# Kernel tuning notes

Hardware: AMD Instinct MI355X
Metric: run time of the kernel (lower is better)

The kernel has to match this reference:

```python
import jax, jax.numpy as jnp
import numpy as np

B, L, C = 32, 2048, 32
PL, STRIDE = 16, 16
P = L // PL
D, H_ENC, H_DEC, K, NH = 64, 256, 256, 512, 4
BETA, EPS, Q_EPS, CW = 0.25, 1e-5, 1e-5, 0.2


def setup_inputs() -> dict:
    key = jax.random.key(0)
    ks = jax.random.split(key, 16)
    g = lambda k, sh: 0.02 * jax.random.normal(k, sh, dtype=jnp.float32)
    return {
        'x': jax.random.normal(ks[0], (B, L, C), dtype=jnp.float32),
        'revin_w': jnp.ones((C,), jnp.float32), 'revin_b': jnp.zeros((C,), jnp.float32),
        'inp_W': g(ks[1], (PL, D)), 'inp_b': jnp.zeros((D,), jnp.float32),
        'Wq': g(ks[2], (D, D)), 'bq': jnp.zeros((D,), jnp.float32),
        'Wk': g(ks[3], (D, D)), 'bk': jnp.zeros((D,), jnp.float32),
        'Wv': g(ks[4], (D, D)), 'bv': jnp.zeros((D,), jnp.float32),
        'Wo': g(ks[5], (D, D)), 'bo': jnp.zeros((D,), jnp.float32),
        'ln1_g': jnp.ones((D,), jnp.float32), 'ln1_b': jnp.zeros((D,), jnp.float32),
        'ffn_W1': g(ks[6], (D, H_ENC)), 'ffn_b1': jnp.zeros((H_ENC,), jnp.float32),
        'ffn_W2': g(ks[7], (H_ENC, D)), 'ffn_b2': jnp.zeros((D,), jnp.float32),
        'ln2_g': jnp.ones((D,), jnp.float32), 'ln2_b': jnp.zeros((D,), jnp.float32),
        'codebook': jax.random.uniform(ks[8], (K, D), jnp.float32, -1.0 / K, 1.0 / K),
        'dec_W1': g(ks[9], (D, H_DEC)), 'dec_b1': jnp.zeros((H_DEC,), jnp.float32),
        'dec_W2': g(ks[10], (H_DEC, PL)), 'dec_b2': jnp.zeros((PL,), jnp.float32),
        'dec_Wr': g(ks[11], (D, PL)), 'dec_br': jnp.zeros((PL,), jnp.float32),
        'dec_ln_g': jnp.ones((PL,), jnp.float32), 'dec_ln_b': jnp.zeros((PL,), jnp.float32),
    }


def _layernorm(x, g, b):
    m = jnp.mean(x, -1, keepdims=True)
    v = jnp.mean((x - m) ** 2, -1, keepdims=True)
    return (x - m) * jax.lax.rsqrt(v + EPS) * g + b


def reference(x, revin_w, revin_b, inp_W, inp_b, Wq, bq, Wk, bk, Wv, bv, Wo, bo,
              ln1_g, ln1_b, ffn_W1, ffn_b1, ffn_W2, ffn_b2, ln2_g, ln2_b, codebook,
              dec_W1, dec_b1, dec_W2, dec_b2, dec_Wr, dec_br, dec_ln_g, dec_ln_b):
    # --- RevIN norm (stats over time dim) ---
    mean = jnp.mean(x, axis=1, keepdims=True)              # [B,1,C]
    std = jnp.sqrt(jnp.var(x, axis=1, keepdims=True) + EPS)
    xn = (x - mean) / std * revin_w + revin_b
    # --- patchify: [B,C,L] -> [B*C, P, PL] ---
    patches = jnp.transpose(xn, (0, 2, 1)).reshape(B * C, P, PL)
    # --- MHEncoder ---
    h = patches @ inp_W + inp_b                            # [N,P,D]
    dh = D // NH
    q = (h @ Wq + bq).reshape(-1, P, NH, dh)
    k = (h @ Wk + bk).reshape(-1, P, NH, dh)
    v = (h @ Wv + bv).reshape(-1, P, NH, dh)
    scores = jnp.einsum('nqhd,nkhd->nhqk', q, k) / np.sqrt(dh).astype(np.float32)
    attn = jax.nn.softmax(scores, axis=-1)
    a = jnp.einsum('nhqk,nkhd->nqhd', attn, v).reshape(-1, P, D)
    a = a @ Wo + bo
    h = _layernorm(h + a, ln1_g, ln1_b)
    ff = jax.nn.relu(h @ ffn_W1 + ffn_b1) @ ffn_W2 + ffn_b2
    h = _layernorm(h + ff, ln2_g, ln2_b)
    z = h.reshape(B, C, P, D)
    # --- ClusterQuantizer ---
    z2 = jnp.sum(z * z, -1, keepdims=True)                 # [B,V,P,1]
    e2 = jnp.sum(codebook * codebook, -1)                  # [K]
    ze = jnp.einsum('bvpd,kd->bvpk', z, codebook)
    dist = z2 + e2 - 2.0 * ze                              # [B,V,P,K]
    indices = jnp.argmin(dist, axis=-1)                    # [B,V,P] int
    z_q = codebook[indices]
    z_q_st = z + jax.lax.stop_gradient(z_q - z)
    codebook_loss = jnp.mean((z_q - jax.lax.stop_gradient(z)) ** 2)
    commitment_loss = jnp.mean((z - jax.lax.stop_gradient(z_q)) ** 2)
    cluster_loss = codebook_loss + BETA * commitment_loss
    counts = jnp.zeros((K,), jnp.float32).at[indices.ravel()].add(1.0)
    probs = counts / (counts.sum() + EPS)
    perplexity = jnp.exp(-jnp.sum(probs * jnp.log(probs + EPS)))
    # --- FFN decoder ---
    y = jax.nn.relu(z_q_st @ dec_W1 + dec_b1) @ dec_W2 + dec_b2
    y = y + z_q_st @ dec_Wr + dec_br
    recon_patches = _layernorm(y, dec_ln_g, dec_ln_b)      # [B,V,P,PL]
    recon = jnp.transpose(recon_patches.reshape(B, C, L), (0, 2, 1))  # [B,L,C]
    # --- RevIN denorm ---
    r = (recon - revin_b) / (revin_w + EPS * EPS) * std + mean
    rec_loss = jnp.mean((x - r) ** 2)
    loss_total = rec_loss + CW * cluster_loss
    return (loss_total, rec_loss, z_q_st, r, indices, perplexity)
```

## Files before the change

### kernel.cpp

```cpp
#include <hip/hip_runtime.h>
#include <math.h>

#define TPB 256

#define B_  32
#define L_  2048
#define C_  32
#define PL_ 16
#define P_  128
#define D_  64
#define HE_ 256
#define HD_ 256
#define K_  512
#define N_  1024
#define M_  131072

#define EPS_  1e-5f
#define BETA_ 0.25f
#define CW_   0.2f

#define OUT_LOSS 0
#define OUT_REC  1
#define OUT_ZQ   2
#define OUT_R    8388610
#define OUT_IDX  10485762
#define OUT_PERP 10616834

#define WS_MEAN   0
#define WS_STD    1024
#define WS_QT     2048
#define WS_KT     6144
#define WS_VT     10240
#define WS_E2     34816
#define WS_COUNTS 35328
#define WS_CPART  35840
#define WS_H0     36864
#define WS_H1     8425472
#define WS_RPART  WS_H1

__global__ void k_prep(const float* __restrict__ Wq, const float* __restrict__ Wk,
                       const float* __restrict__ Wv,
                       const float* __restrict__ cb, float* __restrict__ ws) {
    int g = blockIdx.x * TPB + threadIdx.x;
    if (g < 4096) { int t = g >> 6, j = g & 63; ws[WS_QT + g] = Wq[j * D_ + t]; }
    else if (g < 8192) { int g2 = g - 4096; int t = g2 >> 6, j = g2 & 63; ws[WS_KT + g2] = Wk[j * D_ + t]; }
    else if (g < 12288) { int g2 = g - 8192; int t = g2 >> 6, j = g2 & 63; ws[WS_VT + g2] = Wv[j * D_ + t]; }
    if (g < K_) {
        float s = 0.f;
        for (int j = 0; j < D_; j++) { float v = cb[g * D_ + j]; s += v * v; }
        ws[WS_E2 + g] = s;
    }
}

__global__ void k_stats(const float* __restrict__ x, float* __restrict__ ws) {
    const int blk = blockIdx.x;
    const int b = blk >> 3, c0 = (blk & 7) * 4;
    const float4* xp = (const float4*)(x + (size_t)b * L_ * C_ + c0);
    float4 s = {0.f, 0.f, 0.f, 0.f}, s2 = {0.f, 0.f, 0.f, 0.f};
    for (int l = threadIdx.x; l < L_; l += TPB) {
        float4 v = xp[(size_t)l * 8];
        s.x += v.x; s.y += v.y; s.z += v.z; s.w += v.w;
        s2.x += v.x * v.x; s2.y += v.y * v.y; s2.z += v.z * v.z; s2.w += v.w * v.w;
    }
    __shared__ float4 sh[TPB], sh2[TPB];
    sh[threadIdx.x] = s; sh2[threadIdx.x] = s2; __syncthreads();
    for (int o2 = 128; o2 > 0; o2 >>= 1) {
        if (threadIdx.x < o2) {
            float4 a = sh[threadIdx.x], bq_ = sh[threadIdx.x + o2];
            a.x += bq_.x; a.y += bq_.y; a.z += bq_.z; a.w += bq_.w; sh[threadIdx.x] = a;
            float4 a2 = sh2[threadIdx.x], b2_ = sh2[threadIdx.x + o2];
            a2.x += b2_.x; a2.y += b2_.y; a2.z += b2_.z; a2.w += b2_.w; sh2[threadIdx.x] = a2;
        }
        __syncthreads();
    }
    if (threadIdx.x == 0) {
        float sv[4] = {sh[0].x, sh[0].y, sh[0].z, sh[0].w};
        float qv[4] = {sh2[0].x, sh2[0].y, sh2[0].z, sh2[0].w};
#pragma unroll
        for (int u = 0; u < 4; u++) {
            float m = sv[u] / (float)L_;
            float var = qv[u] / (float)L_ - m * m;
            ws[WS_MEAN + b * 32 + c0 + u] = m;
            ws[WS_STD + b * 32 + c0 + u] = sqrtf(var + EPS_);
        }
    }
}

__global__ __launch_bounds__(TPB) void k_embed(
    const float* __restrict__ x, const float* __restrict__ rw, const float* __restrict__ rb,
    const float* __restrict__ inpW, const float* __restrict__ inpb, float* __restrict__ ws) {
    int g = blockIdx.x * TPB + threadIdx.x;
    int row = g >> 4, d4 = g & 15;
    int n = row >> 7, p = row & 127;
    int b = n >> 5, c = n & 31;
    float m = ws[WS_MEAN + n], sd = ws[WS_STD + n];
    float w = rw[c], bb = rb[c];
    const float* xp = x + (size_t)b * L_ * C_ + (size_t)p * PL_ * C_ + c;
    const float4* W4 = (const float4*)inpW;
    float4 acc = ((const float4*)inpb)[d4];
#pragma unroll
    for (int j = 0; j < PL_; j++) {
        float xv = xp[(size_t)j * C_];
        float xn = (xv - m) / sd * w + bb;
        float4 wv = W4[j * 16 + d4];
        acc.x += xn * wv.x; acc.y += xn * wv.y; acc.z += xn * wv.z; acc.w += xn * wv.w;
    }
    ((float4*)(ws + WS_H0))[g] = acc;
}

#define HSS  68
#define HS_  0
#define KH_  8704
#define VH_  10752
#define SMF  12800

__global__ __launch_bounds__(TPB) void k_attn(
    float* __restrict__ ws,
    const float* __restrict__ bq, const float* __restrict__ bk, const float* __restrict__ bv) {
    __shared__ float sm[SMF];
    const int tid = threadIdx.x;
    const int xcd = blockIdx.x & 7, iw = blockIdx.x >> 3;
    const int n = xcd * 128 + (iw >> 2), hh = iw & 3;
    const float* h0 = ws + WS_H0 + (size_t)n * (P_ * D_);
    float* agl = ws + WS_H1 + (size_t)n * (P_ * D_);

    {
        const float4* h04 = (const float4*)h0;
#pragma unroll
        for (int it = 0; it < 8; ++it) {
            int e = tid + it * 256;
            int r = e >> 4, j4 = e & 15;
            *(float4*)(sm + HS_ + r * HSS + j4 * 4) = h04[e];
        }
    }
    __syncthreads();

    const int t_ = tid & 15, ib = tid >> 4;
    const float4* WqT4 = (const float4*)(ws + WS_QT);
    const float4* WkT4 = (const float4*)(ws + WS_KT);
    const float4* WvT4 = (const float4*)(ws + WS_VT);

    {
        float4 wk[16], wv[16];
        const float4* kr = WkT4 + (size_t)(hh * 16 + t_) * 16;
        const float4* vr = WvT4 + (size_t)(hh * 16 + t_) * 16;
#pragma unroll
        for (int j4 = 0; j4 < 16; j4++) { wk[j4] = kr[j4]; wv[j4] = vr[j4]; }
        float bbk = bk[hh * 16 + t_], bbv = bv[hh * 16 + t_];
#pragma unroll
        for (int it = 0; it < 8; it++) {
            int i2 = ib + it * 16;
            const float4* hr = (const float4*)(sm + HS_ + i2 * HSS);
            float accK = bbk, accV = bbv;
#pragma unroll
            for (int j4 = 0; j4 < 16; j4++) {
                float4 h4 = hr[j4];
                float4 k4 = wk[j4], v4 = wv[j4];
                accK += h4.x * k4.x + h4.y * k4.y + h4.z * k4.z + h4.w * k4.w;
                accV += h4.x * v4.x + h4.y * v4.y + h4.z * v4.z + h4.w * v4.w;
            }
            sm[KH_ + i2 * 16 + t_] = accK;
            sm[VH_ + i2 * 16 + t_] = accV;
        }
    }
    const int rg = tid >> 2, qt = tid & 3;
    const int rmine = qt >> 1, hmine = qt & 1;
    float qA[16], qB[16];
    {
        const int myrow = rg * 2 + rmine;
        float4 hreg[16];
        const float4* hr = (const float4*)(sm + HS_ + myrow * HSS);
#pragma unroll
        for (int j4 = 0; j4 < 16; j4++) hreg[j4] = hr[j4];
        float qh[8];
#pragma unroll
        for (int u = 0; u < 8; u++) {
            const float4* wr = WqT4 + (size_t)(hh * 16 + hmine * 8 + u) * 16;
            float acc = bq[hh * 16 + hmine * 8 + u];
#pragma unroll
            for (int j4 = 0; j4 < 16; j4++) {
                float4 w4 = wr[j4];
                acc += hreg[j4].x * w4.x + hreg[j4].y * w4.y + hreg[j4].z * w4.z + hreg[j4].w * w4.w;
            }
            qh[u] = acc;
        }
        float qm[16];
#pragma unroll
        for (int u = 0; u < 8; u++) {
            float oth = __shfl_xor(qh[u], 1);
            qm[u] = hmine ? oth : qh[u];
            qm[8 + u] = hmine ? qh[u] : oth;
        }
#pragma unroll
        for (int u = 0; u < 16; u++) {
            float oth = __shfl_xor(qm[u], 2);
            qA[u] = rmine ? oth : qm[u];
            qB[u] = rmine ? qm[u] : oth;
        }
    }
    __syncthreads();
    float SA = 0.f, SB = 0.f;
    float oA[16], oB[16];
#pragma unroll
    for (int u = 0; u < 16; u++) { oA[u] = 0.f; oB[u] = 0.f; }
    const float4* kh4 = (const float4*)(sm + KH_);
    const float4* vh4 = (const float4*)(sm + VH_);
#pragma unroll 4
    for (int k = 0; k < 32; k++) {
        int m = k * 4 + qt;
        float4 a0 = kh4[m * 4 + 0], a1 = kh4[m * 4 + 1], a2 = kh4[m * 4 + 2], a3 = kh4[m * 4 + 3];
        float sA = qA[0] * a0.x + qA[1] * a0.y + qA[2] * a0.z + qA[3] * a0.w
                 + qA[4] * a1.x + qA[5] * a1.y + qA[6] * a1.z + qA[7] * a1.w
                 + qA[8] * a2.x + qA[9] * a2.y + qA[10] * a2.z + qA[11] * a2.w
                 + qA[12] * a3.x + qA[13] * a3.y + qA[14] * a3.z + qA[15] * a3.w;
        float sB = qB[0] * a0.x + qB[1] * a0.y + qB[2] * a0.z + qB[3] * a0.w
                 + qB[4] * a1.x + qB[5] * a1.y + qB[6] * a1.z + qB[7] * a1.w
                 + qB[8] * a2.x + qB[9] * a2.y + qB[10] * a2.z + qB[11] * a2.w
                 + qB[12] * a3.x + qB[13] * a3.y + qB[14] * a3.z + qB[15] * a3.w;
        float pA = __expf(sA * 0.25f);
        float pB = __expf(sB * 0.25f);
        SA += pA; SB += pB;
        float4 v0 = vh4[m * 4 + 0], v1 = vh4[m * 4 + 1], v2 = vh4[m * 4 + 2], v3 = vh4[m * 4 + 3];
        oA[0] += pA * v0.x; oA[1] += pA * v0.y; oA[2] += pA * v0.z; oA[3] += pA * v0.w;
        oA[4] += pA * v1.x; oA[5] += pA * v1.y; oA[6] += pA * v1.z; oA[7] += pA * v1.w;
        oA[8] += pA * v2.x; oA[9] += pA * v2.y; oA[10] += pA * v2.z; oA[11] += pA * v2.w;
        oA[12] += pA * v3.x; oA[13] += pA * v3.y; oA[14] += pA * v3.z; oA[15] += pA * v3.w;
        oB[0] += pB * v0.x; oB[1] += pB * v0.y; oB[2] += pB * v0.z; oB[3] += pB * v0.w;
        oB[4] += pB * v1.x; oB[5] += pB * v1.y; oB[6] += pB * v1.z; oB[7] += pB * v1.w;
        oB[8] += pB * v2.x; oB[9] += pB * v2.y; oB[10] += pB * v2.z; oB[11] += pB * v2.w;
        oB[12] += pB * v3.x; oB[13] += pB * v3.y; oB[14] += pB * v3.z; oB[15] += pB * v3.w;
    }
    {
        SA += __shfl_xor(SA, 1); SA += __shfl_xor(SA, 2);
        SB += __shfl_xor(SB, 1); SB += __shfl_xor(SB, 2);
        float invA = 1.f / SA, invB = 1.f / SB;
#pragma unroll
        for (int u = 0; u < 16; u++) {
            oA[u] += __shfl_xor(oA[u], 1); oA[u] += __shfl_xor(oA[u], 2);
            oB[u] += __shfl_xor(oB[u], 1); oB[u] += __shfl_xor(oB[u], 2);
        }
        const int myrow = rg * 2 + rmine;
        float inv = rmine ? invB : invA;
        float wv[8];
#pragma unroll
        for (int u = 0; u < 8; u++) {
            float va = oA[hmine * 8 + u], vb = oB[hmine * 8 + u];
            wv[u] = (rmine ? vb : va) * inv;
        }
        float4 r0, r1;
        r0.x = wv[0]; r0.y = wv[1]; r0.z = wv[2]; r0.w = wv[3];
        r1.x = wv[4]; r1.y = wv[5]; r1.z = wv[6]; r1.w = wv[7];
        float4* ap4 = (float4*)(agl + (size_t)myrow * D_ + hh * 16 + hmine * 8);
        ap4[0] = r0; ap4[1] = r1;
    }
}

#define FHS  68

__global__ __launch_bounds__(TPB) void k_woffn(
    float* __restrict__ ws, const float* __restrict__ Wo, const float* __restrict__ bo,
    const float* __restrict__ g1, const float* __restrict__ b1,
    const float* __restrict__ fW1, const float* __restrict__ fb1,
    const float* __restrict__ fW2, const float* __restrict__ fb2,
    const float* __restrict__ g2, const float* __restrict__ b2) {
    __shared__ float bufA[64][FHS];
    __shared__ float hT[64][FHS];
    const int tid = threadIdx.x;
    const int row0 = blockIdx.x * 64;
    const float* aog = ws + WS_H1 + (size_t)row0 * D_;

    {
        const float4* ao4 = (const float4*)aog;
#pragma unroll
        for (int it = 0; it < 4; ++it) {
            int e = tid + it * 256;
            int r = e >> 4, j4 = e & 15;
            float4 v = ao4[e];
            bufA[j4 * 4 + 0][r] = v.x; bufA[j4 * 4 + 1][r] = v.y;
            bufA[j4 * 4 + 2][r] = v.z; bufA[j4 * 4 + 3][r] = v.w;
        }
    }
    const int ty = tid >> 4, tx = tid & 15;
    float acc[4][4];
    {
        float4 bb = ((const float4*)bo)[tx];
#pragma unroll
        for (int r = 0; r < 4; r++) { acc[r][0] = bb.x; acc[r][1] = bb.y; acc[r][2] = bb.z; acc[r][3] = bb.w; }
    }
    __syncthreads();
    const float4* Wo4 = (const float4*)Wo;
#pragma unroll 4
    for (int j = 0; j < 64; ++j) {
        float4 a = *(const float4*)&bufA[j][ty * 4];
        float4 w = Wo4[j * 16 + tx];
        float ar[4] = {a.x, a.y, a.z, a.w}, wr[4] = {w.x, w.y, w.z, w.w};
#pragma unroll
        for (int r = 0; r < 4; r++)
#pragma unroll
            for (int c = 0; c < 4; c++) acc[r][c] += ar[r] * wr[c];
    }
    float h1v[4][4];
    {
        const float4* h04 = (const float4*)(ws + WS_H0 + (size_t)row0 * D_);
        float4 gg = ((const float4*)g1)[tx], bbn = ((const float4*)b1)[tx];
#pragma unroll
        for (int r = 0; r < 4; r++) {
            float4 res = h04[(ty * 4 + r) * 16 + tx];
            acc[r][0] += res.x; acc[r][1] += res.y; acc[r][2] += res.z; acc[r][3] += res.w;
            float s = acc[r][0] + acc[r][1] + acc[r][2] + acc[r][3];
            s += __shfl_xor(s, 1); s += __shfl_xor(s, 2); s += __shfl_xor(s, 4); s += __shfl_xor(s, 8);
            float mean_ = s * (1.f / 64.f);
            float vv = 0.f;
#pragma unroll
            for (int c = 0; c < 4; c++) { float d_ = acc[r][c] - mean_; vv += d_ * d_; }
            vv += __shfl_xor(vv, 1); vv += __shfl_xor(vv, 2); vv += __shfl_xor(vv, 4); vv += __shfl_xor(vv, 8);
            float rstd = 1.f / sqrtf(vv * (1.f / 64.f) + EPS_);
            h1v[r][0] = (acc[r][0] - mean_) * rstd * gg.x + bbn.x;
            h1v[r][1] = (acc[r][1] - mean_) * rstd * gg.y + bbn.y;
            h1v[r][2] = (acc[r][2] - mean_) * rstd * gg.z + bbn.z;
            h1v[r][3] = (acc[r][3] - mean_) * rstd * gg.w + bbn.w;
        }
    }
#pragma unroll
    for (int r = 0; r < 4; r++)
#pragma unroll
        for (int c = 0; c < 4; c++) hT[tx * 4 + c][ty * 4 + r] = h1v[r][c];
    const float4* W14 = (const float4*)fW1;
    const float4* W24 = (const float4*)fW2;
    float outv[4][4];
    {
        float4 bb = ((const float4*)fb2)[tx];
#pragma unroll
        for (int r = 0; r < 4; r++) { outv[r][0] = bb.x; outv[r][1] = bb.y; outv[r][2] = bb.z; outv[r][3] = bb.w; }
    }
    __syncthreads();

    for (int tc = 0; tc < 4; ++tc) {
        float a2[4][4];
        {
            float4 bb1 = ((const float4*)fb1)[tc * 16 + tx];
#pragma unroll
            for (int r = 0; r < 4; r++) { a2[r][0] = bb1.x; a2[r][1] = bb1.y; a2[r][2] = bb1.z; a2[r][3] = bb1.w; }
        }
#pragma unroll 4
        for (int j = 0; j < 64; ++j) {
            float4 a = *(const float4*)&hT[j][ty * 4];
            float4 w = W14[j * 64 + tc * 16 + tx];
            float ar[4] = {a.x, a.y, a.z, a.w}, wr[4] = {w.x, w.y, w.z, w.w};
#pragma unroll
            for (int r = 0; r < 4; r++)
#pragma unroll
                for (int c = 0; c < 4; c++) a2[r][c] += ar[r] * wr[c];
        }
        __syncthreads();
#pragma unroll
        for (int r = 0; r < 4; r++)
#pragma unroll
            for (int c = 0; c < 4; c++) bufA[tx * 4 + c][ty * 4 + r] = fmaxf(a2[r][c], 0.f);
        __syncthreads();
#pragma unroll 4
        for (int h = 0; h < 64; ++h) {
            float4 a = *(const float4*)&bufA[h][ty * 4];
            float4 w = W24[(tc * 64 + h) * 16 + tx];
            float ar[4] = {a.x, a.y, a.z, a.w}, wr[4] = {w.x, w.y, w.z, w.w};
#pragma unroll
            for (int r = 0; r < 4; r++)
#pragma unroll
                for (int c = 0; c < 4; c++) outv[r][c] += ar[r] * wr[c];
        }
    }
    {
        float4 gg = ((const float4*)g2)[tx], bb = ((const float4*)b2)[tx];
        float4* zp = (float4*)(ws + WS_H0 + (size_t)row0 * D_);
#pragma unroll
        for (int r = 0; r < 4; r++) {
            outv[r][0] += h1v[r][0]; outv[r][1] += h1v[r][1];
            outv[r][2] += h1v[r][2]; outv[r][3] += h1v[r][3];
            float s = outv[r][0] + outv[r][1] + outv[r][2] + outv[r][3];
            s += __shfl_xor(s, 1); s += __shfl_xor(s, 2); s += __shfl_xor(s, 4); s += __shfl_xor(s, 8);
            float mean_ = s * (1.f / 64.f);
            float vv = 0.f;
#pragma unroll
            for (int c = 0; c < 4; c++) { float d_ = outv[r][c] - mean_; vv += d_ * d_; }
            vv += __shfl_xor(vv, 1); vv += __shfl_xor(vv, 2); vv += __shfl_xor(vv, 4); vv += __shfl_xor(vv, 8);
            float rstd = 1.f / sqrtf(vv * (1.f / 64.f) + EPS_);
            float4 z;
            z.x = (outv[r][0] - mean_) * rstd * gg.x + bb.x;
            z.y = (outv[r][1] - mean_) * rstd * gg.y + bb.y;
            z.z = (outv[r][2] - mean_) * rstd * gg.z + bb.z;
            z.w = (outv[r][3] - mean_) * rstd * gg.w + bb.w;
            zp[(ty * 4 + r) * 16 + tx] = z;
        }
    }
}

#define QROWS 128
#define QKT   64
#define ZTS   132
#define CBS   68

__global__ __launch_bounds__(TPB) void k_quant(
    float* __restrict__ ws, const float* __restrict__ cb, float* __restrict__ out) {
    __shared__ float zT[64][ZTS];
    __shared__ float cbT[64][CBS];
    __shared__ float z2s[QROWS];
    __shared__ float e2t[QKT];
    __shared__ int   ridx[QROWS];
    __shared__ float red[TPB];

    const int tid = threadIdx.x;
    const int row0 = blockIdx.x * QROWS;
    const float* zg = ws + WS_H0 + (size_t)row0 * D_;
    const float4* zg4 = (const float4*)zg;
    const float4* cbg4 = (const float4*)cb;

    {
        int j4 = tid >> 4;
#pragma unroll
        for (int it = 0; it < 8; ++it) {
            int r = (tid & 15) + it * 16;
            float4 v = zg4[r * 16 + j4];
            zT[j4 * 4 + 0][r] = v.x; zT[j4 * 4 + 1][r] = v.y;
            zT[j4 * 4 + 2][r] = v.z; zT[j4 * 4 + 3][r] = v.w;
        }
    }
    if (tid < QROWS) {
        const float4* zr = (const float4*)(zg + (size_t)tid * D_);
        float s = 0.f;
#pragma unroll
        for (int j = 0; j < 16; j++) { float4 v = zr[j]; s += v.x * v.x + v.y * v.y + v.z * v.z + v.w * v.w; }
        z2s[tid] = s;
    }

    const int ty = tid >> 4, tx = tid & 15;
    float best[8]; int bidx[8];
#pragma unroll
    for (int u = 0; u < 8; u++) { best[u] = 3.4e38f; bidx[u] = 0; }

    for (int t = 0; t < K_ / QKT; ++t) {
        const int k0 = t * QKT;
        __syncthreads();
        {
            int j4 = tid >> 4;
#pragma unroll
            for (int it = 0; it < 4; ++it) {
                int kk = (tid & 15) + it * 16;
                float4 v = cbg4[(size_t)(k0 + kk) * 16 + j4];
                cbT[j4 * 4 + 0][kk] = v.x; cbT[j4 * 4 + 1][kk] = v.y;
                cbT[j4 * 4 + 2][kk] = v.z; cbT[j4 * 4 + 3][kk] = v.w;
            }
        }
        if (tid < QKT) e2t[tid] = ws[WS_E2 + k0 + tid];
        __syncthreads();

        float acc[8][4];
#pragma unroll
        for (int u = 0; u < 8; u++)
#pragma unroll
            for (int c = 0; c < 4; c++) acc[u][c] = 0.f;

        for (int j = 0; j < 64; ++j) {
            float4 a0 = *(const float4*)&zT[j][ty * 8];
            float4 a1 = *(const float4*)&zT[j][ty * 8 + 4];
            float4 b0 = *(const float4*)&cbT[j][tx * 4];
            float ar[8] = {a0.x, a0.y, a0.z, a0.w, a1.x, a1.y, a1.z, a1.w};
            float br[4] = {b0.x, b0.y, b0.z, b0.w};
#pragma unroll
            for (int u = 0; u < 8; u++)
#pragma unroll
                for (int c = 0; c < 4; c++) acc[u][c] += ar[u] * br[c];
        }

#pragma unroll
        for (int u = 0; u < 8; u++) {
            float z2v = z2s[ty * 8 + u];
#pragma unroll
            for (int c = 0; c < 4; c++) {
                float dist = (z2v + e2t[tx * 4 + c]) - 2.f * acc[u][c];
                int kidx = k0 + tx * 4 + c;
                if (dist < best[u]) { best[u] = dist; bidx[u] = kidx; }
            }
        }
    }

#pragma unroll
    for (int m = 1; m <= 8; m <<= 1) {
#pragma unroll
        for (int u = 0; u < 8; u++) {
            float ob = __shfl_xor(best[u], m, 64);
            int oi = __shfl_xor(bidx[u], m, 64);
            if (ob < best[u] || (ob == best[u] && oi < bidx[u])) { best[u] = ob; bidx[u] = oi; }
        }
    }
    if (tx == 0) {
#pragma unroll
        for (int u = 0; u < 8; u++) ridx[ty * 8 + u] = bidx[u];
    }
    __syncthreads();

    if (tid < QROWS) {
        int bi = ridx[tid];
        out[OUT_IDX + row0 + tid] = (float)bi;
        atomicAdd((unsigned int*)ws + WS_COUNTS + bi, 1u);
    }
    {
        int r = tid >> 1, half = tid & 1;
        int bi = ridx[r];
        const float4* cw = (const float4*)(cb + (size_t)bi * D_ + half * 32);
        const float4* zr4 = (const float4*)(zg + (size_t)r * D_ + half * 32);
        float2* zqo = (float2*)(out + OUT_ZQ + (size_t)(row0 + r) * D_ + half * 32);
        float csum = 0.f;
#pragma unroll
        for (int j4 = 0; j4 < 8; ++j4) {
            float4 w = cw[j4]; float4 zz = zr4[j4];
            float d0 = w.x - zz.x, d1 = w.y - zz.y, d2 = w.z - zz.z, d3 = w.w - zz.w;
            csum += d0 * d0 + d1 * d1 + d2 * d2 + d3 * d3;
            float2 p0; p0.x = w.x; p0.y = w.y; zqo[j4 * 2] = p0;
            float2 p1; p1.x = w.z; p1.y = w.w; zqo[j4 * 2 + 1] = p1;
        }
        red[tid] = csum;
    }
    __syncthreads();
    for (int o2 = 128; o2 > 0; o2 >>= 1) {
        if (tid < o2) red[tid] += red[tid + o2];
        __syncthreads();
    }
    if (tid == 0) ws[WS_CPART + blockIdx.x] = red[0];
}

#define DR_ 64

__global__ __launch_bounds__(TPB) void k_dec(
    float* __restrict__ ws, const float* __restrict__ x, const float* __restrict__ cb,
    const float* __restrict__ dW1, const float* __restrict__ db1,
    const float* __restrict__ dW2, const float* __restrict__ db2,
    const float* __restrict__ dWr, const float* __restrict__ dbr,
    const float* __restrict__ lng, const float* __restrict__ lnb,
    const float* __restrict__ rw, const float* __restrict__ rb,
    float* __restrict__ out) {
    __shared__ float zqT[64][FHS];
    __shared__ float Hc[64][FHS];
    __shared__ int   ridx[DR_];
    __shared__ float red[TPB];
    const int tid = threadIdx.x;
    const int row0 = blockIdx.x * DR_;
    if (tid < DR_) ridx[tid] = (int)out[OUT_IDX + row0 + tid];
    __syncthreads();
    {
        const float4* cb4 = (const float4*)cb;
#pragma unroll
        for (int it = 0; it < 4; ++it) {
            int e = tid + it * 256;
            int r = e >> 4, j4 = e & 15;
            float4 v = cb4[(size_t)ridx[r] * 16 + j4];
            zqT[j4 * 4 + 0][r] = v.x; zqT[j4 * 4 + 1][r] = v.y;
            zqT[j4 * 4 + 2][r] = v.z; zqT[j4 * 4 + 3][r] = v.w;
        }
    }
    const int ty = tid >> 4, tx = tid & 15;
    const float4* dW14 = (const float4*)dW1;
    float out4[4];
    {
        float b0 = db2[tx] + dbr[tx];
#pragma unroll
        for (int r = 0; r < 4; r++) out4[r] = b0;
    }
    __syncthreads();

    for (int tc = 0; tc < 4; ++tc) {
        float acc[4][4];
        {
            float4 bb1 = ((const float4*)db1)[tc * 16 + tx];
#pragma unroll
            for (int r = 0; r < 4; r++) { acc[r][0] = bb1.x; acc[r][1] = bb1.y; acc[r][2] = bb1.z; acc[r][3] = bb1.w; }
        }
#pragma unroll 4
        for (int j = 0; j < 64; ++j) {
            float4 a = *(const float4*)&zqT[j][ty * 4];
            float4 w = dW14[j * 64 + tc * 16 + tx];
            float ar[4] = {a.x, a.y, a.z, a.w}, wr[4] = {w.x, w.y, w.z, w.w};
#pragma unroll
            for (int r = 0; r < 4; r++)
#pragma unroll
                for (int c = 0; c < 4; c++) acc[r][c] += ar[r] * wr[c];
        }
        __syncthreads();
#pragma unroll
        for (int r = 0; r < 4; r++)
#pragma unroll
            for (int c = 0; c < 4; c++) Hc[tx * 4 + c][ty * 4 + r] = fmaxf(acc[r][c], 0.f);
        __syncthreads();
#pragma unroll 8
        for (int h = 0; h < 64; ++h) {
            float4 a = *(const float4*)&Hc[h][ty * 4];
            float w = dW2[(tc * 64 + h) * 16 + tx];
            out4[0] += a.x * w; out4[1] += a.y * w; out4[2] += a.z * w; out4[3] += a.w * w;
        }
    }
#pragma unroll 8
    for (int j = 0; j < 64; ++j) {
        float4 a = *(const float4*)&zqT[j][ty * 4];
        float w = dWr[j * 16 + tx];
        out4[0] += a.x * w; out4[1] += a.y * w; out4[2] += a.z * w; out4[3] += a.w * w;
    }
    const int n = row0 >> 7;
    const int b = n >> 5, c = n & 31;
    const float sd = ws[WS_STD + n], mn = ws[WS_MEAN + n];
    const float inv = 1.f / (rw[c] + EPS_ * EPS_);
    const float rbc = rb[c];
    const float lg = lng[tx], lb = lnb[tx];
    float part = 0.f;
#pragma unroll
    for (int r = 0; r < 4; r++) {
        float v = out4[r];
        float s = v;
        s += __shfl_xor(s, 1); s += __shfl_xor(s, 2); s += __shfl_xor(s, 4); s += __shfl_xor(s, 8);
        float mean_ = s * (1.f / 16.f);
        float d_ = v - mean_;
        float vv = d_ * d_;
        vv += __shfl_xor(vv, 1); vv += __shfl_xor(vv, 2); vv += __shfl_xor(vv, 4); vv += __shfl_xor(vv, 8);
        float rstd = 1.f / sqrtf(vv * (1.f / 16.f) + EPS_);
        float yv = d_ * rstd * lg + lb;
        float rr = (yv - rbc) * inv * sd + mn;
        int row = row0 + ty * 4 + r;
        int p = row & 127;
        size_t xi = (size_t)b * L_ * C_ + (size_t)(p * PL_ + tx) * C_ + c;
        out[OUT_R + xi] = rr;
        float dx = x[xi] - rr; part += dx * dx;
    }
    red[tid] = part;
    __syncthreads();
    for (int o2 = 128; o2 > 0; o2 >>= 1) {
        if (tid < o2) red[tid] += red[tid + o2];
        __syncthreads();
    }
    if (tid == 0) ws[WS_RPART + blockIdx.x] = red[0];
}

__global__ void k_final(float* __restrict__ ws, float* __restrict__ out) {
    __shared__ float sh[TPB];
    int tid = threadIdx.x;
    float cs = 0.f;
    for (int i2 = tid; i2 < 1024; i2 += TPB) cs += ws[WS_CPART + i2];
    sh[tid] = cs; __syncthreads();
    for (int o2 = 128; o2 > 0; o2 >>= 1) { if (tid < o2) sh[tid] += sh[tid + o2]; __syncthreads(); }
    float csum = sh[0]; __syncthreads();
    float rs = 0.f;
    for (int i2 = tid; i2 < 2048; i2 += TPB) rs += ws[WS_RPART + i2];
    sh[tid] = rs; __syncthreads();
    for (int o2 = 128; o2 > 0; o2 >>= 1) { if (tid < o2) sh[tid] += sh[tid + o2]; __syncthreads(); }
    float rsum = sh[0]; __syncthreads();
    const unsigned int* counts = (const unsigned int*)ws + WS_COUNTS;
    float H = 0.f;
    for (int k2 = tid; k2 < K_; k2 += TPB) {
        float p = (float)counts[k2] / (131072.f + EPS_);
        H += p * logf(p + EPS_);
    }
    sh[tid] = H; __syncthreads();
    for (int o2 = 128; o2 > 0; o2 >>= 1) { if (tid < o2) sh[tid] += sh[tid + o2]; __syncthreads(); }
    if (tid == 0) {
        float rec = rsum / 2097152.f;
        float msd = csum / 8388608.f;
        float cl = (1.f + BETA_) * msd;
        out[OUT_LOSS] = rec + CW_ * cl;
        out[OUT_REC] = rec;
        out[OUT_PERP] = expf(-sh[0]);
    }
}

extern "C" void kernel_launch(void* const* d_in, const int* in_sizes, int n_in,
                              void* d_out, int out_size, void* d_ws, size_t ws_size,
                              hipStream_t stream) {
    const float* x    = (const float*)d_in[0];
    const float* rw   = (const float*)d_in[1];
    const float* rb   = (const float*)d_in[2];
    const float* inpW = (const float*)d_in[3];
    const float* inpb = (const float*)d_in[4];
    const float* Wq   = (const float*)d_in[5];
    const float* bq   = (const float*)d_in[6];
    const float* Wk   = (const float*)d_in[7];
    const float* bk   = (const float*)d_in[8];
    const float* Wv   = (const float*)d_in[9];
    const float* bv   = (const float*)d_in[10];
    const float* Wo   = (const float*)d_in[11];
    const float* bo   = (const float*)d_in[12];
    const float* g1   = (const float*)d_in[13];
    const float* b1   = (const float*)d_in[14];
    const float* fW1  = (const float*)d_in[15];
    const float* fb1  = (const float*)d_in[16];
    const float* fW2  = (const float*)d_in[17];
    const float* fb2  = (const float*)d_in[18];
    const float* g2   = (const float*)d_in[19];
    const float* b2   = (const float*)d_in[20];
    const float* cb   = (const float*)d_in[21];
    const float* dW1  = (const float*)d_in[22];
    const float* db1  = (const float*)d_in[23];
    const float* dW2  = (const float*)d_in[24];
    const float* db2  = (const float*)d_in[25];
    const float* dWr  = (const float*)d_in[26];
    const float* dbr  = (const float*)d_in[27];
    const float* lng  = (const float*)d_in[28];
    const float* lnb  = (const float*)d_in[29];
    float* ws  = (float*)d_ws;
    float* out = (float*)d_out;

    hipMemsetAsync((char*)d_ws + (size_t)WS_COUNTS * 4, 0, 512 * 4, stream);
    k_prep<<<48, TPB, 0, stream>>>(Wq, Wk, Wv, cb, ws);
    k_stats<<<256, TPB, 0, stream>>>(x, ws);
    k_embed<<<(M_ * 16) / TPB, TPB, 0, stream>>>(x, rw, rb, inpW, inpb, ws);
    k_attn<<<N_ * 4, TPB, 0, stream>>>(ws, bq, bk, bv);
    k_woffn<<<M_ / 64, TPB, 0, stream>>>(ws, Wo, bo, g1, b1, fW1, fb1, fW2, fb2, g2, b2);
    k_quant<<<M_ / QROWS, TPB, 0, stream>>>(ws, cb, out);
    k_dec<<<M_ / DR_, TPB, 0, stream>>>(ws, x, cb, dW1, db1, dW2, db2, dWr, dbr, lng, lnb, rw, rb, out);
    k_final<<<1, TPB, 0, stream>>>(ws, out);
}
```

Baseline: 660.0 us.

## Fuse vector quantization into Wo/FFN kernel and process two heads per attention block

Vector quantization now runs at the end of the Wo/FFN/LayerNorm kernel. The normalized z is kept transposed in shared memory and its squared norms are computed in registers, so z is no longer written to global memory and read back by a separate quant kernel. Each attention block now handles two heads in a loop, so the staged h0 tile in shared memory is reused and half as many blocks are launched. The fused quant uses 64-row tiles, so the codebook is streamed twice as often in total. Codebook-loss partials move to the now-unused transposed-Wq workspace region, and the final reduction sums 2048 partials.

```diff
diff --git a/kernel.cpp b/kernel.cpp
--- a/kernel.cpp
+++ b/kernel.cpp
@@ -33,10 +33,10 @@
 #define WS_VT     10240
 #define WS_E2     34816
 #define WS_COUNTS 35328
-#define WS_CPART  35840
 #define WS_H0     36864
 #define WS_H1     8425472
 #define WS_RPART  WS_H1
+#define WS_CPART2 WS_QT
 
 __global__ void k_prep(const float* __restrict__ Wq, const float* __restrict__ Wk,
                        const float* __restrict__ Wv,
@@ -120,7 +120,7 @@
     __shared__ float sm[SMF];
     const int tid = threadIdx.x;
     const int xcd = blockIdx.x & 7, iw = blockIdx.x >> 3;
-    const int n = xcd * 128 + (iw >> 2), hh = iw & 3;
+    const int n = xcd * 128 + (iw >> 1), hp = iw & 1;
     const float* h0 = ws + WS_H0 + (size_t)n * (P_ * D_);
     float* agl = ws + WS_H1 + (size_t)n * (P_ * D_);
 
@@ -136,135 +136,142 @@
     __syncthreads();
 
     const int t_ = tid & 15, ib = tid >> 4;
+    const int rg = tid >> 2, qt = tid & 3;
+    const int rmine = qt >> 1, hmine = qt & 1;
     const float4* WqT4 = (const float4*)(ws + WS_QT);
     const float4* WkT4 = (const float4*)(ws + WS_KT);
     const float4* WvT4 = (const float4*)(ws + WS_VT);
 
-    {
-        float4 wk[16], wv[16];
-        const float4* kr = WkT4 + (size_t)(hh * 16 + t_) * 16;
-        const float4* vr = WvT4 + (size_t)(hh * 16 + t_) * 16;
-#pragma unroll
-        for (int j4 = 0; j4 < 16; j4++) { wk[j4] = kr[j4]; wv[j4] = vr[j4]; }
-        float bbk = bk[hh * 16 + t_], bbv = bv[hh * 16 + t_];
-#pragma unroll
-        for (int it = 0; it < 8; it++) {
-            int i2 = ib + it * 16;
-            const float4* hr = (const float4*)(sm + HS_ + i2 * HSS);
-            float accK = bbk, accV = bbv;
-#pragma unroll
-            for (int j4 = 0; j4 < 16; j4++) {
-                float4 h4 = hr[j4];
-                float4 k4 = wk[j4], v4 = wv[j4];
-                accK += h4.x * k4.x + h4.y * k4.y + h4.z * k4.z + h4.w * k4.w;
-                accV += h4.x * v4.x + h4.y * v4.y + h4.z * v4.z + h4.w * v4.w;
-            }
-            sm[KH_ + i2 * 16 + t_] = accK;
-            sm[VH_ + i2 * 16 + t_] = accV;
-        }
-    }
-    const int rg = tid >> 2, qt = tid & 3;
-    const int rmine = qt >> 1, hmine = qt & 1;
-    float qA[16], qB[16];
-    {
-        const int myrow = rg * 2 + rmine;
-        float4 hreg[16];
-        const float4* hr = (const float4*)(sm + HS_ + myrow * HSS);
-#pragma unroll
-        for (int j4 = 0; j4 < 16; j4++) hreg[j4] = hr[j4];
-        float qh[8];
-#pragma unroll
-        for (int u = 0; u < 8; u++) {
-            const float4* wr = WqT4 + (size_t)(hh * 16 + hmine * 8 + u) * 16;
-            float acc = bq[hh * 16 + hmine * 8 + u];
-#pragma unroll
-            for (int j4 = 0; j4 < 16; j4++) {
-                float4 w4 = wr[j4];
-                acc += hreg[j4].x * w4.x + hreg[j4].y * w4.y + hreg[j4].z * w4.z + hreg[j4].w * w4.w;
-            }
-            qh[u] = acc;
-        }
-        float qm[16];
-#pragma unroll
-        for (int u = 0; u < 8; u++) {
-            float oth = __shfl_xor(qh[u], 1);
-            qm[u] = hmine ? oth : qh[u];
-            qm[8 + u] = hmine ? qh[u] : oth;
-        }
-#pragma unroll
-        for (int u = 0; u < 16; u++) {
-            float oth = __shfl_xor(qm[u], 2);
-            qA[u] = rmine ? oth : qm[u];
-            qB[u] = rmine ? qm[u] : oth;
-        }
-    }
-    __syncthreads();
-    float SA = 0.f, SB = 0.f;
-    float oA[16], oB[16];
-#pragma unroll
-    for (int u = 0; u < 16; u++) { oA[u] = 0.f; oB[u] = 0.f; }
-    const float4* kh4 = (const float4*)(sm + KH_);
-    const float4* vh4 = (const float4*)(sm + VH_);
+    for (int hl = 0; hl < 2; hl++) {
+        const int hh = hp * 2 + hl;
+        if (hl) __syncthreads();
+        {
+            float4 wk[16], wv[16];
+            const float4* kr = WkT4 + (size_t)(hh * 16 + t_) * 16;
+            const float4* vr = WvT4 + (size_t)(hh * 16 + t_) * 16;
+#pragma unroll
+            for (int j4 = 0; j4 < 16; j4++) { wk[j4] = kr[j4]; wv[j4] = vr[j4]; }
+            float bbk = bk[hh * 16 + t_], bbv = bv[hh * 16 + t_];
+#pragma unroll
+            for (int it = 0; it < 8; it++) {
+                int i2 = ib + it * 16;
+                const float4* hr = (const float4*)(sm + HS_ + i2 * HSS);
+                float accK = bbk, accV = bbv;
+#pragma unroll
+                for (int j4 = 0; j4 < 16; j4++) {
+                    float4 h4 = hr[j4];
+                    float4 k4 = wk[j4], v4 = wv[j4];
+                    accK += h4.x * k4.x + h4.y * k4.y + h4.z * k4.z + h4.w * k4.w;
+                    accV += h4.x * v4.x + h4.y * v4.y + h4.z * v4.z + h4.w * v4.w;
+                }
+                sm[KH_ + i2 * 16 + t_] = accK;
+                sm[VH_ + i2 * 16 + t_] = accV;
+            }
+        }
+        float qA[16], qB[16];
+        {
+            const int myrow = rg * 2 + rmine;
+            float4 hreg[16];
+            const float4* hr = (const float4*)(sm + HS_ + myrow * HSS);
+#pragma unroll
+            for (int j4 = 0; j4 < 16; j4++) hreg[j4] = hr[j4];
+            float qh[8];
+#pragma unroll
+            for (int u = 0; u < 8; u++) {
+                const float4* wr = WqT4 + (size_t)(hh * 16 + hmine * 8 + u) * 16;
+                float acc = bq[hh * 16 + hmine * 8 + u];
+#pragma unroll
+                for (int j4 = 0; j4 < 16; j4++) {
+                    float4 w4 = wr[j4];
+                    acc += hreg[j4].x * w4.x + hreg[j4].y * w4.y + hreg[j4].z * w4.z + hreg[j4].w * w4.w;
+                }
+                qh[u] = acc;
+            }
+            float qm[16];
+#pragma unroll
+            for (int u = 0; u < 8; u++) {
+                float oth = __shfl_xor(qh[u], 1);
+                qm[u] = hmine ? oth : qh[u];
+                qm[8 + u] = hmine ? qh[u] : oth;
+            }
+#pragma unroll
+            for (int u = 0; u < 16; u++) {
+                float oth = __shfl_xor(qm[u], 2);
+                qA[u] = rmine ? oth : qm[u];
+                qB[u] = rmine ? qm[u] : oth;
+            }
+        }
+        __syncthreads();
+        float SA = 0.f, SB = 0.f;
+        float oA[16], oB[16];
+#pragma unroll
+        for (int u = 0; u < 16; u++) { oA[u] = 0.f; oB[u] = 0.f; }
+        const float4* kh4 = (const float4*)(sm + KH_);
+        const float4* vh4 = (const float4*)(sm + VH_);
 #pragma unroll 4
-    for (int k = 0; k < 32; k++) {
-        int m = k * 4 + qt;
-        float4 a0 = kh4[m * 4 + 0], a1 = kh4[m * 4 + 1], a2 = kh4[m * 4 + 2], a3 = kh4[m * 4 + 3];
-        float sA = qA[0] * a0.x + qA[1] * a0.y + qA[2] * a0.z + qA[3] * a0.w
-                 + qA[4] * a1.x + qA[5] * a1.y + qA[6] * a1.z + qA[7] * a1.w
-                 + qA[8] * a2.x + qA[9] * a2.y + qA[10] * a2.z + qA[11] * a2.w
-                 + qA[12] * a3.x + qA[13] * a3.y + qA[14] * a3.z + qA[15] * a3.w;
-        float sB = qB[0] * a0.x + qB[1] * a0.y + qB[2] * a0.z + qB[3] * a0.w
-                 + qB[4] * a1.x + qB[5] * a1.y + qB[6] * a1.z + qB[7] * a1.w
-                 + qB[8] * a2.x + qB[9] * a2.y + qB[10] * a2.z + qB[11] * a2.w
-                 + qB[12] * a3.x + qB[13] * a3.y + qB[14] * a3.z + qB[15] * a3.w;
-        float pA = __expf(sA * 0.25f);
-        float pB = __expf(sB * 0.25f);
-        SA += pA; SB += pB;
-        float4 v0 = vh4[m * 4 + 0], v1 = vh4[m * 4 + 1], v2 = vh4[m * 4 + 2], v3 = vh4[m * 4 + 3];
-        oA[0] += pA * v0.x; oA[1] += pA * v0.y; oA[2] += pA * v0.z; oA[3] += pA * v0.w;
-        oA[4] += pA * v1.x; oA[5] += pA * v1.y; oA[6] += pA * v1.z; oA[7] += pA * v1.w;
-        oA[8] += pA * v2.x; oA[9] += pA * v2.y; oA[10] += pA * v2.z; oA[11] += pA * v2.w;
-        oA[12] += pA * v3.x; oA[13] += pA * v3.y; oA[14] += pA * v3.z; oA[15] += pA * v3.w;
-        oB[0] += pB * v0.x; oB[1] += pB * v0.y; oB[2] += pB * v0.z; oB[3] += pB * v0.w;
-        oB[4] += pB * v1.x; oB[5] += pB * v1.y; oB[6] += pB * v1.z; oB[7] += pB * v1.w;
-        oB[8] += pB * v2.x; oB[9] += pB * v2.y; oB[10] += pB * v2.z; oB[11] += pB * v2.w;
-        oB[12] += pB * v3.x; oB[13] += pB * v3.y; oB[14] += pB * v3.z; oB[15] += pB * v3.w;
-    }
-    {
-        SA += __shfl_xor(SA, 1); SA += __shfl_xor(SA, 2);
-        SB += __shfl_xor(SB, 1); SB += __shfl_xor(SB, 2);
-        float invA = 1.f / SA, invB = 1.f / SB;
-#pragma unroll
-        for (int u = 0; u < 16; u++) {
-            oA[u] += __shfl_xor(oA[u], 1); oA[u] += __shfl_xor(oA[u], 2);
-            oB[u] += __shfl_xor(oB[u], 1); oB[u] += __shfl_xor(oB[u], 2);
-        }
-        const int myrow = rg * 2 + rmine;
-        float inv = rmine ? invB : invA;
-        float wv[8];
-#pragma unroll
-        for (int u = 0; u < 8; u++) {
-            float va = oA[hmine * 8 + u], vb = oB[hmine * 8 + u];
-            wv[u] = (rmine ? vb : va) * inv;
-        }
-        float4 r0, r1;
-        r0.x = wv[0]; r0.y = wv[1]; r0.z = wv[2]; r0.w = wv[3];
-        r1.x = wv[4]; r1.y = wv[5]; r1.z = wv[6]; r1.w = wv[7];
-        float4* ap4 = (float4*)(agl + (size_t)myrow * D_ + hh * 16 + hmine * 8);
-        ap4[0] = r0; ap4[1] = r1;
+        for (int k = 0; k < 32; k++) {
+            int m = k * 4 + qt;
+            float4 a0 = kh4[m * 4 + 0], a1 = kh4[m * 4 + 1], a2 = kh4[m * 4 + 2], a3 = kh4[m * 4 + 3];
+            float sA = qA[0] * a0.x + qA[1] * a0.y + qA[2] * a0.z + qA[3] * a0.w
+                     + qA[4] * a1.x + qA[5] * a1.y + qA[6] * a1.z + qA[7] * a1.w
+                     + qA[8] * a2.x + qA[9] * a2.y + qA[10] * a2.z + qA[11] * a2.w
+                     + qA[12] * a3.x + qA[13] * a3.y + qA[14] * a3.z + qA[15] * a3.w;
+            float sB = qB[0] * a0.x + qB[1] * a0.y + qB[2] * a0.z + qB[3] * a0.w
+                     + qB[4] * a1.x + qB[5] * a1.y + qB[6] * a1.z + qB[7] * a1.w
+                     + qB[8] * a2.x + qB[9] * a2.y + qB[10] * a2.z + qB[11] * a2.w
+                     + qB[12] * a3.x + qB[13] * a3.y + qB[14] * a3.z + qB[15] * a3.w;
+            float pA = __expf(sA * 0.25f);
+            float pB = __expf(sB * 0.25f);
+            SA += pA; SB += pB;
+            float4 v0 = vh4[m * 4 + 0], v1 = vh4[m * 4 + 1], v2 = vh4[m * 4 + 2], v3 = vh4[m * 4 + 3];
+            oA[0] += pA * v0.x; oA[1] += pA * v0.y; oA[2] += pA * v0.z; oA[3] += pA * v0.w;
+            oA[4] += pA * v1.x; oA[5] += pA * v1.y; oA[6] += pA * v1.z; oA[7] += pA * v1.w;
+            oA[8] += pA * v2.x; oA[9] += pA * v2.y; oA[10] += pA * v2.z; oA[11] += pA * v2.w;
+            oA[12] += pA * v3.x; oA[13] += pA * v3.y; oA[14] += pA * v3.z; oA[15] += pA * v3.w;
+            oB[0] += pB * v0.x; oB[1] += pB * v0.y; oB[2] += pB * v0.z; oB[3] += pB * v0.w;
+            oB[4] += pB * v1.x; oB[5] += pB * v1.y; oB[6] += pB * v1.z; oB[7] += pB * v1.w;
+            oB[8] += pB * v2.x; oB[9] += pB * v2.y; oB[10] += pB * v2.z; oB[11] += pB * v2.w;
+            oB[12] += pB * v3.x; oB[13] += pB * v3.y; oB[14] += pB * v3.z; oB[15] += pB * v3.w;
+        }
+        {
+            SA += __shfl_xor(SA, 1); SA += __shfl_xor(SA, 2);
+            SB += __shfl_xor(SB, 1); SB += __shfl_xor(SB, 2);
+            float invA = 1.f / SA, invB = 1.f / SB;
+#pragma unroll
+            for (int u = 0; u < 16; u++) {
+                oA[u] += __shfl_xor(oA[u], 1); oA[u] += __shfl_xor(oA[u], 2);
+                oB[u] += __shfl_xor(oB[u], 1); oB[u] += __shfl_xor(oB[u], 2);
+            }
+            const int myrow = rg * 2 + rmine;
+            float inv = rmine ? invB : invA;
+            float wv[8];
+#pragma unroll
+            for (int u = 0; u < 8; u++) {
+                float va = oA[hmine * 8 + u], vb = oB[hmine * 8 + u];
+                wv[u] = (rmine ? vb : va) * inv;
+            }
+            float4 r0, r1;
+            r0.x = wv[0]; r0.y = wv[1]; r0.z = wv[2]; r0.w = wv[3];
+            r1.x = wv[4]; r1.y = wv[5]; r1.z = wv[6]; r1.w = wv[7];
+            float4* ap4 = (float4*)(agl + (size_t)myrow * D_ + hh * 16 + hmine * 8);
+            ap4[0] = r0; ap4[1] = r1;
+        }
     }
 }
 
 #define FHS  68
 
-__global__ __launch_bounds__(TPB) void k_woffn(
+__global__ __launch_bounds__(TPB) void k_wfq(
     float* __restrict__ ws, const float* __restrict__ Wo, const float* __restrict__ bo,
     const float* __restrict__ g1, const float* __restrict__ b1,
     const float* __restrict__ fW1, const float* __restrict__ fb1,
     const float* __restrict__ fW2, const float* __restrict__ fb2,
-    const float* __restrict__ g2, const float* __restrict__ b2) {
+    const float* __restrict__ g2, const float* __restrict__ b2,
+    const float* __restrict__ cb, float* __restrict__ out) {
     __shared__ float bufA[64][FHS];
     __shared__ float hT[64][FHS];
+    __shared__ int   ridx[64];
+    __shared__ float red[TPB];
     const int tid = threadIdx.x;
     const int row0 = blockIdx.x * 64;
     const float* aog = ws + WS_H1 + (size_t)row0 * D_;
@@ -369,9 +376,9 @@
                 for (int c = 0; c < 4; c++) outv[r][c] += ar[r] * wr[c];
         }
     }
+    float z2r[4];
     {
         float4 gg = ((const float4*)g2)[tx], bb = ((const float4*)b2)[tx];
-        float4* zp = (float4*)(ws + WS_H0 + (size_t)row0 * D_);
 #pragma unroll
         for (int r = 0; r < 4; r++) {
             outv[r][0] += h1v[r][0]; outv[r][1] += h1v[r][1];
@@ -384,61 +391,26 @@
             for (int c = 0; c < 4; c++) { float d_ = outv[r][c] - mean_; vv += d_ * d_; }
             vv += __shfl_xor(vv, 1); vv += __shfl_xor(vv, 2); vv += __shfl_xor(vv, 4); vv += __shfl_xor(vv, 8);
             float rstd = 1.f / sqrtf(vv * (1.f / 64.f) + EPS_);
-            float4 z;
-            z.x = (outv[r][0] - mean_) * rstd * gg.x + bb.x;
-            z.y = (outv[r][1] - mean_) * rstd * gg.y + bb.y;
-            z.z = (outv[r][2] - mean_) * rstd * gg.z + bb.z;
-            z.w = (outv[r][3] - mean_) * rstd * gg.w + bb.w;
-            zp[(ty * 4 + r) * 16 + tx] = z;
-        }
-    }
-}
-
-#define QROWS 128
-#define QKT   64
-#define ZTS   132
-#define CBS   68
-
-__global__ __launch_bounds__(TPB) void k_quant(
-    float* __restrict__ ws, const float* __restrict__ cb, float* __restrict__ out) {
-    __shared__ float zT[64][ZTS];
-    __shared__ float cbT[64][CBS];
-    __shared__ float z2s[QROWS];
-    __shared__ float e2t[QKT];
-    __shared__ int   ridx[QROWS];
-    __shared__ float red[TPB];
-
-    const int tid = threadIdx.x;
-    const int row0 = blockIdx.x * QROWS;
-    const float* zg = ws + WS_H0 + (size_t)row0 * D_;
-    const float4* zg4 = (const float4*)zg;
+            float z0 = (outv[r][0] - mean_) * rstd * gg.x + bb.x;
+            float z1 = (outv[r][1] - mean_) * rstd * gg.y + bb.y;
+            float z2_ = (outv[r][2] - mean_) * rstd * gg.z + bb.z;
+            float z3 = (outv[r][3] - mean_) * rstd * gg.w + bb.w;
+            hT[tx * 4 + 0][ty * 4 + r] = z0;
+            hT[tx * 4 + 1][ty * 4 + r] = z1;
+            hT[tx * 4 + 2][ty * 4 + r] = z2_;
+            hT[tx * 4 + 3][ty * 4 + r] = z3;
+            float zs = z0 * z0 + z1 * z1 + z2_ * z2_ + z3 * z3;
+            zs += __shfl_xor(zs, 1); zs += __shfl_xor(zs, 2); zs += __shfl_xor(zs, 4); zs += __shfl_xor(zs, 8);
+            z2r[r] = zs;
+        }
+    }
     const float4* cbg4 = (const float4*)cb;
-
-    {
-        int j4 = tid >> 4;
-#pragma unroll
-        for (int it = 0; it < 8; ++it) {
-            int r = (tid & 15) + it * 16;
-            float4 v = zg4[r * 16 + j4];
-            zT[j4 * 4 + 0][r] = v.x; zT[j4 * 4 + 1][r] = v.y;
-            zT[j4 * 4 + 2][r] = v.z; zT[j4 * 4 + 3][r] = v.w;
-        }
-    }
-    if (tid < QROWS) {
-        const float4* zr = (const float4*)(zg + (size_t)tid * D_);
-        float s = 0.f;
-#pragma unroll
-        for (int j = 0; j < 16; j++) { float4 v = zr[j]; s += v.x * v.x + v.y * v.y + v.z * v.z + v.w * v.w; }
-        z2s[tid] = s;
-    }
-
-    const int ty = tid >> 4, tx = tid & 15;
-    float best[8]; int bidx[8];
-#pragma unroll
-    for (int u = 0; u < 8; u++) { best[u] = 3.4e38f; bidx[u] = 0; }
-
-    for (int t = 0; t < K_ / QKT; ++t) {
-        const int k0 = t * QKT;
+    float best[4]; int bidx[4];
+#pragma unroll
+    for (int u = 0; u < 4; u++) { best[u] = 3.4e38f; bidx[u] = 0; }
+
+    for (int t = 0; t < 8; ++t) {
+        const int k0 = t * 64;
         __syncthreads();
         {
             int j4 = tid >> 4;
@@ -446,47 +418,43 @@
             for (int it = 0; it < 4; ++it) {
                 int kk = (tid & 15) + it * 16;
                 float4 v = cbg4[(size_t)(k0 + kk) * 16 + j4];
-                cbT[j4 * 4 + 0][kk] = v.x; cbT[j4 * 4 + 1][kk] = v.y;
-                cbT[j4 * 4 + 2][kk] = v.z; cbT[j4 * 4 + 3][kk] = v.w;
-            }
-        }
-        if (tid < QKT) e2t[tid] = ws[WS_E2 + k0 + tid];
-        __syncthreads();
-
-        float acc[8][4];
-#pragma unroll
-        for (int u = 0; u < 8; u++)
-#pragma unroll
-            for (int c = 0; c < 4; c++) acc[u][c] = 0.f;
-
+                bufA[j4 * 4 + 0][kk] = v.x; bufA[j4 * 4 + 1][kk] = v.y;
+                bufA[j4 * 4 + 2][kk] = v.z; bufA[j4 * 4 + 3][kk] = v.w;
+            }
+        }
+        float4 e2v = *(const float4*)(ws + WS_E2 + k0 + tx * 4);
+        __syncthreads();
+
+        float dacc[4][4];
+#pragma unroll
+        for (int u = 0; u < 4; u++)
+#pragma unroll
+            for (int c = 0; c < 4; c++) dacc[u][c] = 0.f;
+#pragma unroll 4
         for (int j = 0; j < 64; ++j) {
-            float4 a0 = *(const float4*)&zT[j][ty * 8];
-            float4 a1 = *(const float4*)&zT[j][ty * 8 + 4];
-            float4 b0 = *(const float4*)&cbT[j][tx * 4];
-            float ar[8] = {a0.x, a0.y, a0.z, a0.w, a1.x, a1.y, a1.z, a1.w};
-            float br[4] = {b0.x, b0.y, b0.z, b0.w};
-#pragma unroll
-            for (int u = 0; u < 8; u++)
-#pragma unroll
-                for (int c = 0; c < 4; c++) acc[u][c] += ar[u] * br[c];
-        }
-
-#pragma unroll
-        for (int u = 0; u < 8; u++) {
-            float z2v = z2s[ty * 8 + u];
+            float4 a = *(const float4*)&hT[j][ty * 4];
+            float4 b0 = *(const float4*)&bufA[j][tx * 4];
+            float ar[4] = {a.x, a.y, a.z, a.w}, br[4] = {b0.x, b0.y, b0.z, b0.w};
+#pragma unroll
+            for (int u = 0; u < 4; u++)
+#pragma unroll
+                for (int c = 0; c < 4; c++) dacc[u][c] += ar[u] * br[c];
+        }
+        float e2c[4] = {e2v.x, e2v.y, e2v.z, e2v.w};
+#pragma unroll
+        for (int u = 0; u < 4; u++) {
 #pragma unroll
             for (int c = 0; c < 4; c++) {
-                float dist = (z2v + e2t[tx * 4 + c]) - 2.f * acc[u][c];
+                float dist = (z2r[u] + e2c[c]) - 2.f * dacc[u][c];
                 int kidx = k0 + tx * 4 + c;
                 if (dist < best[u]) { best[u] = dist; bidx[u] = kidx; }
             }
         }
     }
-
 #pragma unroll
     for (int m = 1; m <= 8; m <<= 1) {
 #pragma unroll
-        for (int u = 0; u < 8; u++) {
+        for (int u = 0; u < 4; u++) {
             float ob = __shfl_xor(best[u], m, 64);
             int oi = __shfl_xor(bidx[u], m, 64);
             if (ob < best[u] || (ob == best[u] && oi < bidx[u])) { best[u] = ob; bidx[u] = oi; }
@@ -494,26 +462,29 @@
     }
     if (tx == 0) {
 #pragma unroll
-        for (int u = 0; u < 8; u++) ridx[ty * 8 + u] = bidx[u];
-    }
-    __syncthreads();
-
-    if (tid < QROWS) {
+        for (int u = 0; u < 4; u++) ridx[ty * 4 + u] = bidx[u];
+    }
+    __syncthreads();
+
+    if (tid < 64) {
         int bi = ridx[tid];
         out[OUT_IDX + row0 + tid] = (float)bi;
         atomicAdd((unsigned int*)ws + WS_COUNTS + bi, 1u);
     }
     {
-        int r = tid >> 1, half = tid & 1;
+        int r = tid >> 2, q4 = tid & 3;
         int bi = ridx[r];
-        const float4* cw = (const float4*)(cb + (size_t)bi * D_ + half * 32);
-        const float4* zr4 = (const float4*)(zg + (size_t)r * D_ + half * 32);
-        float2* zqo = (float2*)(out + OUT_ZQ + (size_t)(row0 + r) * D_ + half * 32);
+        const float4* cw = (const float4*)(cb + (size_t)bi * D_ + q4 * 16);
+        float2* zqo = (float2*)(out + OUT_ZQ + (size_t)(row0 + r) * D_ + q4 * 16);
         float csum = 0.f;
 #pragma unroll
-        for (int j4 = 0; j4 < 8; ++j4) {
-            float4 w = cw[j4]; float4 zz = zr4[j4];
-            float d0 = w.x - zz.x, d1 = w.y - zz.y, d2 = w.z - zz.z, d3 = w.w - zz.w;
+        for (int j4 = 0; j4 < 4; ++j4) {
+            float4 w = cw[j4];
+            float z0 = hT[q4 * 16 + j4 * 4 + 0][r];
+            float z1 = hT[q4 * 16 + j4 * 4 + 1][r];
+            float z2_ = hT[q4 * 16 + j4 * 4 + 2][r];
+            float z3 = hT[q4 * 16 + j4 * 4 + 3][r];
+            float d0 = w.x - z0, d1 = w.y - z1, d2 = w.z - z2_, d3 = w.w - z3;
             csum += d0 * d0 + d1 * d1 + d2 * d2 + d3 * d3;
             float2 p0; p0.x = w.x; p0.y = w.y; zqo[j4 * 2] = p0;
             float2 p1; p1.x = w.z; p1.y = w.w; zqo[j4 * 2 + 1] = p1;
@@ -525,7 +496,7 @@
         if (tid < o2) red[tid] += red[tid + o2];
         __syncthreads();
     }
-    if (tid == 0) ws[WS_CPART + blockIdx.x] = red[0];
+    if (tid == 0) ws[WS_CPART2 + blockIdx.x] = red[0];
 }
 
 #define DR_ 64
@@ -641,7 +612,7 @@
     __shared__ float sh[TPB];
     int tid = threadIdx.x;
     float cs = 0.f;
-    for (int i2 = tid; i2 < 1024; i2 += TPB) cs += ws[WS_CPART + i2];
+    for (int i2 = tid; i2 < 2048; i2 += TPB) cs += ws[WS_CPART2 + i2];
     sh[tid] = cs; __syncthreads();
     for (int o2 = 128; o2 > 0; o2 >>= 1) { if (tid < o2) sh[tid] += sh[tid + o2]; __syncthreads(); }
     float csum = sh[0]; __syncthreads();
@@ -708,9 +679,8 @@
     k_prep<<<48, TPB, 0, stream>>>(Wq, Wk, Wv, cb, ws);
     k_stats<<<256, TPB, 0, stream>>>(x, ws);
     k_embed<<<(M_ * 16) / TPB, TPB, 0, stream>>>(x, rw, rb, inpW, inpb, ws);
-    k_attn<<<N_ * 4, TPB, 0, stream>>>(ws, bq, bk, bv);
-    k_woffn<<<M_ / 64, TPB, 0, stream>>>(ws, Wo, bo, g1, b1, fW1, fb1, fW2, fb2, g2, b2);
-    k_quant<<<M_ / QROWS, TPB, 0, stream>>>(ws, cb, out);
+    k_attn<<<N_ * 2, TPB, 0, stream>>>(ws, bq, bk, bv);
+    k_wfq<<<M_ / 64, TPB, 0, stream>>>(ws, Wo, bo, g1, b1, fW1, fb1, fW2, fb2, g2, b2, cb, out);
     k_dec<<<M_ / DR_, TPB, 0, stream>>>(ws, x, cb, dW1, db1, dW2, db2, dWr, dbr, lng, lnb, rw, rb, out);
     k_final<<<1, TPB, 0, stream>>>(ws, out);
 }
```

Result: slower. 733.5 us (+11.1%).
